# Optimization experiments

Measured on AMD Instinct MI355X. Metric: run time of the kernel, lower is better.

The kernel has to match this reference:

```python
import jax, jax.numpy as jnp
import numpy as np

EPS = 1e-8  # torch cosine_similarity eps


def setup_inputs() -> dict:
    key = jax.random.key(0)
    kx, kw = jax.random.split(key)
    B, D, C, K = 512, 512, 5994, 3
    x = jax.random.normal(kx, (B, D), dtype=jnp.float32)
    # xavier_normal over (D, C, K): std = sqrt(2 / (fan_in + fan_out))
    std = float(np.sqrt(2.0 / (D + C * K)))
    W = jax.random.normal(kw, (D, C, K), dtype=jnp.float32) * std
    return {"x": x, "W": W}


def reference(x, W):
    # cosine similarity along feature dim, without materializing [B, D, C, K]
    x_norm = jnp.maximum(jnp.linalg.norm(x, axis=1, keepdims=True), EPS)   # [B, 1]
    w_norm = jnp.maximum(jnp.linalg.norm(W, axis=0, keepdims=True), EPS)   # [1, C, K]
    xn = x / x_norm                                                        # [B, D]
    Wn = W / w_norm                                                        # [D, C, K]
    costh = jnp.einsum('bd,dck->bck', xn, Wn)                              # [B, C, K]
    return costh
```

## Files before the change

kernel.cpp:

```cpp
#include <hip/hip_runtime.h>
#include <hip/hip_bf16.h>
#include <stdint.h>


#define D_DIM 512
#define BM 128
#define BN 128
#define KITERS 16
#define TILE_BYTES (64 * BM * 16)

typedef __bf16 bf16x8 __attribute__((ext_vector_type(8)));
typedef __bf16 bf16x2 __attribute__((ext_vector_type(2)));
typedef float f32x4 __attribute__((ext_vector_type(4)));

__device__ __forceinline__ unsigned pk(float a, float b) {
  bf16x2 t; t[0] = (__bf16)a; t[1] = (__bf16)b;
  return __builtin_bit_cast(unsigned, t);
}

__device__ __forceinline__ void load_lds16(const void* g, void* l) {
  __builtin_amdgcn_global_load_lds(
      (__attribute__((address_space(1))) void*)(g),
      (__attribute__((address_space(3))) void*)(l), 16, 0, 0);
}

__global__ void prep_kernel(const float* __restrict__ x, const float* __restrict__ W,
                            unsigned short* __restrict__ An, unsigned short* __restrict__ Wt,
                            float* __restrict__ partial, int CK, int NT128, int nWtBlocks) {
  const int b = blockIdx.x;
  const int t = threadIdx.x;
  if (b < nWtBlocks) {
    __shared__ float red[8 * 128];
    const int ntile = b >> 3, gb = b & 7;
    const int cq = t & 31, dr = t >> 5;
    const int n0 = ntile * BN;
    const int nb = n0 + cq * 4;
    const int g = gb * 8 + dr;
    float ss0 = 0.f, ss1 = 0.f, ss2 = 0.f, ss3 = 0.f;
    unsigned int gr[4][4];
    if (n0 + BN <= CK) {
#pragma unroll
      for (int i = 0; i < 8; i += 2) {
        float4 v0 = *(const float4*)(W + (size_t)(g * 8 + i) * CK + nb);
        float4 v1 = *(const float4*)(W + (size_t)(g * 8 + i + 1) * CK + nb);
        ss0 += v0.x * v0.x + v1.x * v1.x; ss1 += v0.y * v0.y + v1.y * v1.y;
        ss2 += v0.z * v0.z + v1.z * v1.z; ss3 += v0.w * v0.w + v1.w * v1.w;
        gr[0][i >> 1] = pk(v0.x, v1.x);
        gr[1][i >> 1] = pk(v0.y, v1.y);
        gr[2][i >> 1] = pk(v0.z, v1.z);
        gr[3][i >> 1] = pk(v0.w, v1.w);
      }
    } else {
      float acc_ss[4] = {0.f, 0.f, 0.f, 0.f};
#pragma unroll
      for (int i = 0; i < 8; i += 2) {
#pragma unroll
        for (int e = 0; e < 4; ++e) {
          const int n = nb + e;
          const float f0 = (n < CK) ? W[(size_t)(g * 8 + i) * CK + n] : 0.f;
          const float f1 = (n < CK) ? W[(size_t)(g * 8 + i + 1) * CK + n] : 0.f;
          acc_ss[e] += f0 * f0 + f1 * f1;
          gr[e][i >> 1] = pk(f0, f1);
        }
      }
      ss0 = acc_ss[0]; ss1 = acc_ss[1]; ss2 = acc_ss[2]; ss3 = acc_ss[3];
    }
    unsigned short* dst = Wt + (size_t)ntile * (TILE_BYTES / 2) + (size_t)g * (BM * 8) + (size_t)cq * 32;
#pragma unroll
    for (int e = 0; e < 4; ++e) {
      uint4 o; o.x = gr[e][0]; o.y = gr[e][1]; o.z = gr[e][2]; o.w = gr[e][3];
      *(uint4*)(dst + e * 8) = o;
    }
    *(float4*)(&red[dr * 128 + cq * 4]) = make_float4(ss0, ss1, ss2, ss3);
    __syncthreads();
    if (t < 128) {
      float s = 0.f;
#pragma unroll
      for (int k = 0; k < 8; ++k) s += red[k * 128 + t];
      partial[(size_t)gb * NT128 + n0 + t] = s;
    }
  } else {
    const int w = t >> 6, lane = t & 63;
    const int m = (b - nWtBlocks) * 4 + w;
    const float* xr = x + (size_t)m * D_DIM + lane * 8;
    float4 a = *(const float4*)(xr);
    float4 c = *(const float4*)(xr + 4);
    float s = a.x * a.x + a.y * a.y + a.z * a.z + a.w * a.w +
              c.x * c.x + c.y * c.y + c.z * c.z + c.w * c.w;
#pragma unroll
    for (int off = 32; off; off >>= 1) s += __shfl_xor(s, off, 64);
    const float inv = 1.f / fmaxf(sqrtf(s), 1e-8f);
    ushort4 o0, o1;
    const unsigned p0 = pk(a.x * inv, a.y * inv), p1 = pk(a.z * inv, a.w * inv);
    const unsigned p2 = pk(c.x * inv, c.y * inv), p3 = pk(c.z * inv, c.w * inv);
    o0.x = (unsigned short)(p0 & 0xffff); o0.y = (unsigned short)(p0 >> 16);
    o0.z = (unsigned short)(p1 & 0xffff); o0.w = (unsigned short)(p1 >> 16);
    o1.x = (unsigned short)(p2 & 0xffff); o1.y = (unsigned short)(p2 >> 16);
    o1.z = (unsigned short)(p3 & 0xffff); o1.w = (unsigned short)(p3 >> 16);
    const int mtile = m >> 7, r = m & 127;
    unsigned short* dst = An + (size_t)mtile * (TILE_BYTES / 2) + (size_t)lane * (BM * 8) + r * 8;
    *(ushort4*)dst = o0;
    *(ushort4*)(dst + 4) = o1;
  }
}

__global__ __launch_bounds__(256, 3) void gemm_kernel(const unsigned short* __restrict__ An,
                                                      const unsigned short* __restrict__ Wt,
                                                      const float* __restrict__ partial,
                                                      float* __restrict__ out, int CK, int NT128) {
  __shared__ __attribute__((aligned(16))) unsigned char lds[49152];
  const int total = gridDim.x;
  const int q = total >> 3, rr = total & 7;
  const int lin = blockIdx.x;
  const int xcd = lin & 7, idx = lin >> 3;
  const int wg = ((xcd < rr) ? xcd * (q + 1) : rr * (q + 1) + (xcd - rr) * q) + idx;
  const int ntile = wg >> 2, mtile = wg & 3;

  const int t = threadIdx.x;
  const int lane = t & 63, w = t >> 6;
  const int wm = w >> 1, wn = w & 1;
  const int lrow = lane & 15;
  const int kg = lane >> 4;

  const unsigned char* srcA = (const unsigned char*)An + (size_t)mtile * TILE_BYTES;
  const unsigned char* srcB = (const unsigned char*)Wt + (size_t)ntile * TILE_BYTES;
  const int n0 = ntile * BN;
  const bool full = (n0 + BN <= CK);

  f32x4 acc[4][4] = {};

#define STAGE(kt, sel)                                                        \
  {                                                                           \
    const size_t koff = (size_t)(kt) * 8192;                                  \
    unsigned char* bAw = lds + (sel) * 16384;                                 \
    unsigned char* bBw = bAw + 8192;                                          \
    _Pragma("unroll")                                                         \
    for (int c = 0; c < 2; ++c) {                                             \
      const int off = c * 4096 + t * 16;                                      \
      load_lds16(srcA + koff + off, bAw + off);                               \
    }                                                                         \
    _Pragma("unroll")                                                         \
    for (int c = 0; c < 2; ++c) {                                             \
      const int off = c * 4096 + t * 16;                                      \
      load_lds16(srcB + koff + off, bBw + off);                               \
    }                                                                         \
  }

  STAGE(0, 0);
  STAGE(1, 1);

#pragma unroll
  for (int kt = 0; kt < KITERS; ++kt) {
    __builtin_amdgcn_sched_barrier(0);
    if (kt + 1 < KITERS) {
      asm volatile("s_waitcnt vmcnt(4)" ::: "memory");
    } else {
      asm volatile("s_waitcnt vmcnt(0)" ::: "memory");
    }
    __builtin_amdgcn_s_barrier();
    __builtin_amdgcn_sched_barrier(0);

    if (kt + 2 < KITERS) STAGE(kt + 2, (kt + 2) % 3);

    const unsigned char* bA = lds + (kt % 3) * 16384;
    const unsigned char* bB = bA + 8192;
    bf16x8 afrag[4], bfrag[4];
#pragma unroll
    for (int i = 0; i < 4; ++i) {
      afrag[i] = *(const bf16x8*)(bA + kg * 2048 + (wm * 64 + i * 16 + lrow) * 16);
      bfrag[i] = *(const bf16x8*)(bB + kg * 2048 + (wn * 64 + i * 16 + lrow) * 16);
    }
#pragma unroll
    for (int i = 0; i < 4; ++i)
#pragma unroll
      for (int j = 0; j < 4; ++j)
        acc[i][j] = __builtin_amdgcn_mfma_f32_16x16x32_bf16(afrag[i], bfrag[j], acc[i][j], 0, 0, 0);
  }

  __syncthreads();
  float* winv = (float*)lds;
  if (t < 128) {
    float s = 0.f;
#pragma unroll
    for (int k = 0; k < 8; ++k) s += partial[(size_t)k * NT128 + n0 + t];
    winv[t] = 1.f / fmaxf(sqrtf(s), 1e-8f);
  }
  __syncthreads();
  float wv[4];
#pragma unroll
  for (int j = 0; j < 4; ++j) wv[j] = winv[wn * 64 + j * 16 + lrow];

  if (full) {
    float* stg = (float*)(lds + 1024) + w * 2176;
    const int l15 = lane & 15, l4 = lane >> 4;
#pragma unroll
    for (int half = 0; half < 2; ++half) {
#pragma unroll
      for (int di = 0; di < 2; ++di)
#pragma unroll
        for (int j = 0; j < 4; ++j)
#pragma unroll
          for (int jj = 0; jj < 4; ++jj)
            stg[(di * 16 + kg * 4 + jj) * 68 + j * 16 + lrow] = acc[half * 2 + di][j][jj] * wv[j];
#pragma unroll
      for (int s = 0; s < 8; ++s) {
        const int rl = s * 4 + l4;
        float4 v = *(float4*)&stg[rl * 68 + l15 * 4];
        const int row = mtile * BM + wm * 64 + half * 32 + rl;
        *(float4*)&out[(size_t)row * CK + n0 + wn * 64 + l15 * 4] = v;
      }
    }
  } else {
#pragma unroll
    for (int j = 0; j < 4; ++j) {
      const int col = n0 + wn * 64 + j * 16 + lrow;
      if (col < CK) {
#pragma unroll
        for (int i = 0; i < 4; ++i)
#pragma unroll
          for (int jj = 0; jj < 4; ++jj) {
            const int row = mtile * BM + wm * 64 + i * 16 + kg * 4 + jj;
            out[(size_t)row * CK + col] = acc[i][j][jj] * wv[j];
          }
      }
    }
  }
#undef STAGE
}

extern "C" void kernel_launch(void* const* d_in, const int* in_sizes, int n_in,
                              void* d_out, int out_size, void* d_ws, size_t ws_size,
                              hipStream_t stream) {
  const float* x = (const float*)d_in[0];
  const float* W = (const float*)d_in[1];
  float* out = (float*)d_out;
  const int Bn = in_sizes[0] / D_DIM;
  const int CK = in_sizes[1] / D_DIM;
  const int ntiles = (CK + BN - 1) / BN;
  const int mtiles = Bn / BM;
  const int NT128 = ntiles * BN;

  unsigned char* ws = (unsigned char*)d_ws;
  float* partial = (float*)ws;
  unsigned short* An = (unsigned short*)(ws + 8 * (size_t)NT128 * 4);
  unsigned short* Wt = (unsigned short*)(ws + 8 * (size_t)NT128 * 4 + (size_t)mtiles * TILE_BYTES);

  const int nWtBlocks = ntiles * 8;
  const int nXBlocks = Bn / 4;
  hipLaunchKernelGGL(prep_kernel, dim3(nWtBlocks + nXBlocks), dim3(256), 0, stream,
                     x, W, An, Wt, partial, CK, NT128, nWtBlocks);
  hipLaunchKernelGGL(gemm_kernel, dim3(ntiles * mtiles), dim3(256), 0, stream,
                     An, Wt, partial, out, CK, NT128);
}
```

Measured before the change: 37.04 us.

## Load MFMA fragments directly from global into registers, bypassing LDS

The GEMM mainloop stops staging A and B tiles through a triple-buffered LDS ring with global_load_lds, waitcnt and barriers. Each lane now reads its bf16x8 fragments straight from the pre-swizzled global layout into a double-buffered register set, prefetching the next k-step while issuing MFMAs. This removes the LDS round-trip and the per-iteration workgroup barriers. In exchange, warps that share rows or columns now load the same data from global/L2 redundantly, and register pressure rises. The LDS array is shrunk since it is now only used in the epilogue.

```diff
diff --git a/kernel.cpp b/kernel.cpp
--- a/kernel.cpp
+++ b/kernel.cpp
@@ -16,12 +16,6 @@
 __device__ __forceinline__ unsigned pk(float a, float b) {
   bf16x2 t; t[0] = (__bf16)a; t[1] = (__bf16)b;
   return __builtin_bit_cast(unsigned, t);
-}
-
-__device__ __forceinline__ void load_lds16(const void* g, void* l) {
-  __builtin_amdgcn_global_load_lds(
-      (__attribute__((address_space(1))) void*)(g),
-      (__attribute__((address_space(3))) void*)(l), 16, 0, 0);
 }
 
 __global__ void prep_kernel(const float* __restrict__ x, const float* __restrict__ W,
@@ -108,7 +102,7 @@
                                                       const unsigned short* __restrict__ Wt,
                                                       const float* __restrict__ partial,
                                                       float* __restrict__ out, int CK, int NT128) {
-  __shared__ __attribute__((aligned(16))) unsigned char lds[49152];
+  __shared__ __attribute__((aligned(16))) unsigned char lds[36864];
   const int total = gridDim.x;
   const int q = total >> 3, rr = total & 7;
   const int lin = blockIdx.x;
@@ -122,62 +116,42 @@
   const int lrow = lane & 15;
   const int kg = lane >> 4;
 
-  const unsigned char* srcA = (const unsigned char*)An + (size_t)mtile * TILE_BYTES;
-  const unsigned char* srcB = (const unsigned char*)Wt + (size_t)ntile * TILE_BYTES;
+  const unsigned char* pa = (const unsigned char*)An + (size_t)mtile * TILE_BYTES
+                            + kg * 2048 + (wm * 64 + lrow) * 16;
+  const unsigned char* pb = (const unsigned char*)Wt + (size_t)ntile * TILE_BYTES
+                            + kg * 2048 + (wn * 64 + lrow) * 16;
   const int n0 = ntile * BN;
   const bool full = (n0 + BN <= CK);
 
   f32x4 acc[4][4] = {};
-
-#define STAGE(kt, sel)                                                        \
+  bf16x8 fa[2][4], fb[2][4];
+
+#define LOADSET(s, P_A, P_B)                                                  \
   {                                                                           \
-    const size_t koff = (size_t)(kt) * 8192;                                  \
-    unsigned char* bAw = lds + (sel) * 16384;                                 \
-    unsigned char* bBw = bAw + 8192;                                          \
     _Pragma("unroll")                                                         \
-    for (int c = 0; c < 2; ++c) {                                             \
-      const int off = c * 4096 + t * 16;                                      \
-      load_lds16(srcA + koff + off, bAw + off);                               \
-    }                                                                         \
+    for (int i = 0; i < 4; ++i) fa[s][i] = *(const bf16x8*)((P_A) + i * 256); \
     _Pragma("unroll")                                                         \
-    for (int c = 0; c < 2; ++c) {                                             \
-      const int off = c * 4096 + t * 16;                                      \
-      load_lds16(srcB + koff + off, bBw + off);                               \
-    }                                                                         \
-  }
-
-  STAGE(0, 0);
-  STAGE(1, 1);
+    for (int i = 0; i < 4; ++i) fb[s][i] = *(const bf16x8*)((P_B) + i * 256); \
+  }
+
+  LOADSET(0, pa, pb);
 
 #pragma unroll
   for (int kt = 0; kt < KITERS; ++kt) {
-    __builtin_amdgcn_sched_barrier(0);
+    const int s = kt & 1;
     if (kt + 1 < KITERS) {
-      asm volatile("s_waitcnt vmcnt(4)" ::: "memory");
-    } else {
-      asm volatile("s_waitcnt vmcnt(0)" ::: "memory");
-    }
-    __builtin_amdgcn_s_barrier();
-    __builtin_amdgcn_sched_barrier(0);
-
-    if (kt + 2 < KITERS) STAGE(kt + 2, (kt + 2) % 3);
-
-    const unsigned char* bA = lds + (kt % 3) * 16384;
-    const unsigned char* bB = bA + 8192;
-    bf16x8 afrag[4], bfrag[4];
-#pragma unroll
-    for (int i = 0; i < 4; ++i) {
-      afrag[i] = *(const bf16x8*)(bA + kg * 2048 + (wm * 64 + i * 16 + lrow) * 16);
-      bfrag[i] = *(const bf16x8*)(bB + kg * 2048 + (wn * 64 + i * 16 + lrow) * 16);
+      const unsigned char* na = pa + (size_t)(kt + 1) * 8192;
+      const unsigned char* nb = pb + (size_t)(kt + 1) * 8192;
+      LOADSET(s ^ 1, na, nb);
     }
 #pragma unroll
     for (int i = 0; i < 4; ++i)
 #pragma unroll
       for (int j = 0; j < 4; ++j)
-        acc[i][j] = __builtin_amdgcn_mfma_f32_16x16x32_bf16(afrag[i], bfrag[j], acc[i][j], 0, 0, 0);
-  }
-
-  __syncthreads();
+        acc[i][j] = __builtin_amdgcn_mfma_f32_16x16x32_bf16(fa[s][i], fb[s][j], acc[i][j], 0, 0, 0);
+  }
+#undef LOADSET
+
   float* winv = (float*)lds;
   if (t < 128) {
     float s = 0.f;
@@ -225,7 +199,6 @@
       }
     }
   }
-#undef STAGE
 }
 
 extern "C" void kernel_launch(void* const* d_in, const int* in_sizes, int n_in,
```

Result: slower. 39.13 us (+5.6%).

## Fuse prep and GEMM into one persistent kernel with atomic readiness flags

Applied to the files above, without the earlier changes.

Merges the normalization/packing prep kernel and the bf16 MFMA GEMM into a single persistent kernel with a fixed grid of 768 blocks. Blocks first loop over prep work units and signal completion through per-tile atomic counters in workspace. The first nTiles blocks then spin on those counters before running their GEMM tile. This removes the kernel-to-kernel boundary and lets GEMM tiles start once their inputs are ready, at the cost of an extra memset for the flags and spin-wait polling. It also shortens the LDS prefetch from two stages ahead to one, and relies on all 768 blocks being co-resident to avoid deadlock.

```diff
diff --git a/kernel.cpp b/kernel.cpp
--- a/kernel.cpp
+++ b/kernel.cpp
@@ -8,6 +8,7 @@
 #define BN 128
 #define KITERS 16
 #define TILE_BYTES (64 * BM * 16)
+#define GRID 768
 
 typedef __bf16 bf16x8 __attribute__((ext_vector_type(8)));
 typedef __bf16 bf16x2 __attribute__((ext_vector_type(2)));
@@ -24,99 +25,118 @@
       (__attribute__((address_space(3))) void*)(l), 16, 0, 0);
 }
 
-__global__ void prep_kernel(const float* __restrict__ x, const float* __restrict__ W,
-                            unsigned short* __restrict__ An, unsigned short* __restrict__ Wt,
-                            float* __restrict__ partial, int CK, int NT128, int nWtBlocks) {
-  const int b = blockIdx.x;
+__global__ __launch_bounds__(256, 3) void fused_kernel(
+    const float* __restrict__ x, const float* __restrict__ W,
+    unsigned short* __restrict__ An, unsigned short* __restrict__ Wt,
+    float* __restrict__ partial, int* __restrict__ flags,
+    float* __restrict__ out, int CK, int NT128, int nTiles,
+    int nXUnits, int nUnits) {
+  __shared__ __attribute__((aligned(16))) unsigned char lds[49152];
   const int t = threadIdx.x;
-  if (b < nWtBlocks) {
-    __shared__ float red[8 * 128];
-    const int ntile = b >> 3, gb = b & 7;
-    const int cq = t & 31, dr = t >> 5;
-    const int n0 = ntile * BN;
-    const int nb = n0 + cq * 4;
-    const int g = gb * 8 + dr;
-    float ss0 = 0.f, ss1 = 0.f, ss2 = 0.f, ss3 = 0.f;
-    unsigned int gr[4][4];
-    if (n0 + BN <= CK) {
-#pragma unroll
-      for (int i = 0; i < 8; i += 2) {
-        float4 v0 = *(const float4*)(W + (size_t)(g * 8 + i) * CK + nb);
-        float4 v1 = *(const float4*)(W + (size_t)(g * 8 + i + 1) * CK + nb);
-        ss0 += v0.x * v0.x + v1.x * v1.x; ss1 += v0.y * v0.y + v1.y * v1.y;
-        ss2 += v0.z * v0.z + v1.z * v1.z; ss3 += v0.w * v0.w + v1.w * v1.w;
-        gr[0][i >> 1] = pk(v0.x, v1.x);
-        gr[1][i >> 1] = pk(v0.y, v1.y);
-        gr[2][i >> 1] = pk(v0.z, v1.z);
-        gr[3][i >> 1] = pk(v0.w, v1.w);
+  const int bid = blockIdx.x;
+  int* fw = flags;
+  int* fx = flags + 192;
+
+  for (int u = bid; u < nUnits; u += GRID) {
+    if (u < nXUnits) {
+      const int w = t >> 6, lane = t & 63;
+      const int m = u * 4 + w;
+      const float* xr = x + (size_t)m * D_DIM + lane * 8;
+      float4 a = *(const float4*)(xr);
+      float4 c = *(const float4*)(xr + 4);
+      float s = a.x * a.x + a.y * a.y + a.z * a.z + a.w * a.w +
+                c.x * c.x + c.y * c.y + c.z * c.z + c.w * c.w;
+#pragma unroll
+      for (int off = 32; off; off >>= 1) s += __shfl_xor(s, off, 64);
+      const float inv = 1.f / fmaxf(sqrtf(s), 1e-8f);
+      ushort4 o0, o1;
+      const unsigned p0 = pk(a.x * inv, a.y * inv), p1 = pk(a.z * inv, a.w * inv);
+      const unsigned p2 = pk(c.x * inv, c.y * inv), p3 = pk(c.z * inv, c.w * inv);
+      o0.x = (unsigned short)(p0 & 0xffff); o0.y = (unsigned short)(p0 >> 16);
+      o0.z = (unsigned short)(p1 & 0xffff); o0.w = (unsigned short)(p1 >> 16);
+      o1.x = (unsigned short)(p2 & 0xffff); o1.y = (unsigned short)(p2 >> 16);
+      o1.z = (unsigned short)(p3 & 0xffff); o1.w = (unsigned short)(p3 >> 16);
+      const int mtile = m >> 7, r = m & 127;
+      unsigned short* dst = An + (size_t)mtile * (TILE_BYTES / 2) + (size_t)lane * (BM * 8) + r * 8;
+      *(ushort4*)dst = o0;
+      *(ushort4*)(dst + 4) = o1;
+      __syncthreads();
+      if (t == 0) {
+        __threadfence();
+        atomicAdd(&fx[u >> 5], 1);
       }
     } else {
-      float acc_ss[4] = {0.f, 0.f, 0.f, 0.f};
-#pragma unroll
-      for (int i = 0; i < 8; i += 2) {
-#pragma unroll
-        for (int e = 0; e < 4; ++e) {
-          const int n = nb + e;
-          const float f0 = (n < CK) ? W[(size_t)(g * 8 + i) * CK + n] : 0.f;
-          const float f1 = (n < CK) ? W[(size_t)(g * 8 + i + 1) * CK + n] : 0.f;
-          acc_ss[e] += f0 * f0 + f1 * f1;
-          gr[e][i >> 1] = pk(f0, f1);
+      float* red = (float*)lds;
+      const int v = u - nXUnits;
+      const int ntile = v >> 3, gb = v & 7;
+      const int cq = t & 31, dr = t >> 5;
+      const int n0 = ntile * BN;
+      const int nb = n0 + cq * 4;
+      const int g = gb * 8 + dr;
+      float ss0 = 0.f, ss1 = 0.f, ss2 = 0.f, ss3 = 0.f;
+      unsigned int gr[4][4];
+      if (n0 + BN <= CK) {
+#pragma unroll
+        for (int i = 0; i < 8; i += 2) {
+          float4 v0 = *(const float4*)(W + (size_t)(g * 8 + i) * CK + nb);
+          float4 v1 = *(const float4*)(W + (size_t)(g * 8 + i + 1) * CK + nb);
+          ss0 += v0.x * v0.x + v1.x * v1.x; ss1 += v0.y * v0.y + v1.y * v1.y;
+          ss2 += v0.z * v0.z + v1.z * v1.z; ss3 += v0.w * v0.w + v1.w * v1.w;
+          gr[0][i >> 1] = pk(v0.x, v1.x);
+          gr[1][i >> 1] = pk(v0.y, v1.y);
+          gr[2][i >> 1] = pk(v0.z, v1.z);
+          gr[3][i >> 1] = pk(v0.w, v1.w);
         }
-      }
-      ss0 = acc_ss[0]; ss1 = acc_ss[1]; ss2 = acc_ss[2]; ss3 = acc_ss[3];
-    }
-    unsigned short* dst = Wt + (size_t)ntile * (TILE_BYTES / 2) + (size_t)g * (BM * 8) + (size_t)cq * 32;
-#pragma unroll
-    for (int e = 0; e < 4; ++e) {
-      uint4 o; o.x = gr[e][0]; o.y = gr[e][1]; o.z = gr[e][2]; o.w = gr[e][3];
-      *(uint4*)(dst + e * 8) = o;
-    }
-    *(float4*)(&red[dr * 128 + cq * 4]) = make_float4(ss0, ss1, ss2, ss3);
-    __syncthreads();
-    if (t < 128) {
-      float s = 0.f;
-#pragma unroll
-      for (int k = 0; k < 8; ++k) s += red[k * 128 + t];
-      partial[(size_t)gb * NT128 + n0 + t] = s;
-    }
-  } else {
-    const int w = t >> 6, lane = t & 63;
-    const int m = (b - nWtBlocks) * 4 + w;
-    const float* xr = x + (size_t)m * D_DIM + lane * 8;
-    float4 a = *(const float4*)(xr);
-    float4 c = *(const float4*)(xr + 4);
-    float s = a.x * a.x + a.y * a.y + a.z * a.z + a.w * a.w +
-              c.x * c.x + c.y * c.y + c.z * c.z + c.w * c.w;
-#pragma unroll
-    for (int off = 32; off; off >>= 1) s += __shfl_xor(s, off, 64);
-    const float inv = 1.f / fmaxf(sqrtf(s), 1e-8f);
-    ushort4 o0, o1;
-    const unsigned p0 = pk(a.x * inv, a.y * inv), p1 = pk(a.z * inv, a.w * inv);
-    const unsigned p2 = pk(c.x * inv, c.y * inv), p3 = pk(c.z * inv, c.w * inv);
-    o0.x = (unsigned short)(p0 & 0xffff); o0.y = (unsigned short)(p0 >> 16);
-    o0.z = (unsigned short)(p1 & 0xffff); o0.w = (unsigned short)(p1 >> 16);
-    o1.x = (unsigned short)(p2 & 0xffff); o1.y = (unsigned short)(p2 >> 16);
-    o1.z = (unsigned short)(p3 & 0xffff); o1.w = (unsigned short)(p3 >> 16);
-    const int mtile = m >> 7, r = m & 127;
-    unsigned short* dst = An + (size_t)mtile * (TILE_BYTES / 2) + (size_t)lane * (BM * 8) + r * 8;
-    *(ushort4*)dst = o0;
-    *(ushort4*)(dst + 4) = o1;
-  }
-}
-
-__global__ __launch_bounds__(256, 3) void gemm_kernel(const unsigned short* __restrict__ An,
-                                                      const unsigned short* __restrict__ Wt,
-                                                      const float* __restrict__ partial,
-                                                      float* __restrict__ out, int CK, int NT128) {
-  __shared__ __attribute__((aligned(16))) unsigned char lds[49152];
-  const int total = gridDim.x;
-  const int q = total >> 3, rr = total & 7;
-  const int lin = blockIdx.x;
-  const int xcd = lin & 7, idx = lin >> 3;
+      } else {
+        float acc_ss[4] = {0.f, 0.f, 0.f, 0.f};
+#pragma unroll
+        for (int i = 0; i < 8; i += 2) {
+#pragma unroll
+          for (int e = 0; e < 4; ++e) {
+            const int n = nb + e;
+            const float f0 = (n < CK) ? W[(size_t)(g * 8 + i) * CK + n] : 0.f;
+            const float f1 = (n < CK) ? W[(size_t)(g * 8 + i + 1) * CK + n] : 0.f;
+            acc_ss[e] += f0 * f0 + f1 * f1;
+            gr[e][i >> 1] = pk(f0, f1);
+          }
+        }
+        ss0 = acc_ss[0]; ss1 = acc_ss[1]; ss2 = acc_ss[2]; ss3 = acc_ss[3];
+      }
+      unsigned short* dst = Wt + (size_t)ntile * (TILE_BYTES / 2) + (size_t)g * (BM * 8) + (size_t)cq * 32;
+#pragma unroll
+      for (int e = 0; e < 4; ++e) {
+        uint4 o; o.x = gr[e][0]; o.y = gr[e][1]; o.z = gr[e][2]; o.w = gr[e][3];
+        *(uint4*)(dst + e * 8) = o;
+      }
+      *(float4*)(&red[dr * 128 + cq * 4]) = make_float4(ss0, ss1, ss2, ss3);
+      __syncthreads();
+      if (t < 128) {
+        float s = 0.f;
+#pragma unroll
+        for (int k = 0; k < 8; ++k) s += red[k * 128 + t];
+        partial[(size_t)gb * NT128 + n0 + t] = s;
+      }
+      __syncthreads();
+      if (t == 0) {
+        __threadfence();
+        atomicAdd(&fw[ntile], 1);
+      }
+    }
+  }
+
+  if (bid >= nTiles) return;
+  const int q = nTiles >> 3, rr = nTiles & 7;
+  const int xcd = bid & 7, idx = bid >> 3;
   const int wg = ((xcd < rr) ? xcd * (q + 1) : rr * (q + 1) + (xcd - rr) * q) + idx;
   const int ntile = wg >> 2, mtile = wg & 3;
 
-  const int t = threadIdx.x;
+  if (t == 0) {
+    while (atomicAdd(&fw[ntile], 0) < 8) __builtin_amdgcn_s_sleep(2);
+    while (atomicAdd(&fx[mtile], 0) < 32) __builtin_amdgcn_s_sleep(2);
+    __threadfence();
+  }
+  __syncthreads();
+
   const int lane = t & 63, w = t >> 6;
   const int wm = w >> 1, wn = w & 1;
   const int lrow = lane & 15;
@@ -147,10 +167,10 @@
   }
 
   STAGE(0, 0);
-  STAGE(1, 1);
 
 #pragma unroll
   for (int kt = 0; kt < KITERS; ++kt) {
+    if (kt + 1 < KITERS) STAGE(kt + 1, (kt + 1) % 3);
     __builtin_amdgcn_sched_barrier(0);
     if (kt + 1 < KITERS) {
       asm volatile("s_waitcnt vmcnt(4)" ::: "memory");
@@ -160,8 +180,6 @@
     __builtin_amdgcn_s_barrier();
     __builtin_amdgcn_sched_barrier(0);
 
-    if (kt + 2 < KITERS) STAGE(kt + 2, (kt + 2) % 3);
-
     const unsigned char* bA = lds + (kt % 3) * 16384;
     const unsigned char* bB = bA + 8192;
     bf16x8 afrag[4], bfrag[4];
@@ -176,6 +194,7 @@
       for (int j = 0; j < 4; ++j)
         acc[i][j] = __builtin_amdgcn_mfma_f32_16x16x32_bf16(afrag[i], bfrag[j], acc[i][j], 0, 0, 0);
   }
+#undef STAGE
 
   __syncthreads();
   float* winv = (float*)lds;
@@ -225,7 +244,6 @@
       }
     }
   }
-#undef STAGE
 }
 
 extern "C" void kernel_launch(void* const* d_in, const int* in_sizes, int n_in,
@@ -239,16 +257,18 @@
   const int ntiles = (CK + BN - 1) / BN;
   const int mtiles = Bn / BM;
   const int NT128 = ntiles * BN;
+  const int nTiles = ntiles * mtiles;
+  const int nXUnits = Bn / 4;
+  const int nUnits = nXUnits + ntiles * 8;
 
   unsigned char* ws = (unsigned char*)d_ws;
-  float* partial = (float*)ws;
-  unsigned short* An = (unsigned short*)(ws + 8 * (size_t)NT128 * 4);
-  unsigned short* Wt = (unsigned short*)(ws + 8 * (size_t)NT128 * 4 + (size_t)mtiles * TILE_BYTES);
-
-  const int nWtBlocks = ntiles * 8;
-  const int nXBlocks = Bn / 4;
-  hipLaunchKernelGGL(prep_kernel, dim3(nWtBlocks + nXBlocks), dim3(256), 0, stream,
-                     x, W, An, Wt, partial, CK, NT128, nWtBlocks);
-  hipLaunchKernelGGL(gemm_kernel, dim3(ntiles * mtiles), dim3(256), 0, stream,
-                     An, Wt, partial, out, CK, NT128);
-}
+  int* flags = (int*)ws;
+  float* partial = (float*)(ws + 1024);
+  unsigned short* An = (unsigned short*)(ws + 1024 + 8 * (size_t)NT128 * 4);
+  unsigned short* Wt = (unsigned short*)(ws + 1024 + 8 * (size_t)NT128 * 4 + (size_t)mtiles * TILE_BYTES);
+
+  hipMemsetAsync(flags, 0, 1024, stream);
+  hipLaunchKernelGGL(fused_kernel, dim3(GRID), dim3(256), 0, stream,
+                     x, W, An, Wt, partial, flags, out, CK, NT128, nTiles,
+                     nXUnits, nUnits);
+}
```

Measured after the change: 114.6 us. 3.09x slower.
